# Kernel tuning notes

Measured on AMD Instinct MI355X. Metric: run time of the kernel, lower is better.

## Reference

```python
import jax, jax.numpy as jnp
import numpy as np

B = 4          # number of systems in batch
N_PER = 2000   # atoms per system (batch ids are sorted, equal-sized groups)
L = 20.0       # cubic cell edge length (Angstrom)
DL = 2.0       # grid resolution (module default)
SIGMA = 1.0    # Gaussian width (module default)
EPS = 1e-6
NORM = 90.0474
NK = int(np.floor(L / DL))  # static k-grid extent = floor(|cell row| / dl) = 10


def setup_inputs() -> dict:
    key = jax.random.key(0)
    k1, k2 = jax.random.split(key)
    r = jax.random.uniform(k1, (B * N_PER, 3), dtype=jnp.float32) * L
    q = jax.random.normal(k2, (B * N_PER, 1), dtype=jnp.float32)
    cell = jnp.tile(jnp.eye(3, dtype=jnp.float32)[None] * L, (B, 1, 1))
    batch = jnp.repeat(jnp.arange(B, dtype=jnp.int64), N_PER)
    return {"q": q, "r": r, "cell": cell, "batch": batch}


def _ewald(q, r, cell):
    twopi = 2.0 * np.pi
    k_sq_max = (twopi / DL) ** 2
    sigma_sq_half = SIGMA ** 2 / 2.0

    # Static integer k-grid n in [-NK, NK]^3, shape (K, 3), K = (2*NK+1)**3
    rng = jnp.arange(-NK, NK + 1, dtype=r.dtype)
    n1, n2, n3 = jnp.meshgrid(rng, rng, rng, indexing='ij')
    nvec = jnp.stack([n1.ravel(), n2.ravel(), n3.ravel()], axis=1)
    # Hemisphere filter: sign of first nonzero component of nvec > 0
    # (origin n==0 is excluded below by the k_sq > 0 mask, matching torch)
    hemi = ((nvec[:, 0] > 0)
            | ((nvec[:, 0] == 0) & (nvec[:, 1] > 0))
            | ((nvec[:, 0] == 0) & (nvec[:, 1] == 0) & (nvec[:, 2] > 0)))

    # Reciprocal lattice G = 2*pi * inv(cell)^T, per system
    G = twopi * jnp.linalg.inv(cell).transpose(0, 2, 1)        # (B, 3, 3)
    kvec = jnp.einsum('kd,bde->bke', nvec, G)                   # (B, K, 3)
    k_sq = jnp.sum(kvec ** 2, axis=-1)                          # (B, K)
    mask = (k_sq > 0) & (k_sq <= k_sq_max) & hemi[None, :]      # (B, K)

    kfac = jnp.exp(-sigma_sq_half * k_sq) / (k_sq + EPS)        # (B, K)

    pos_b = r.reshape(B, N_PER, 3)
    q_b = q.reshape(B, N_PER)

    kdr = jnp.einsum('bnd,bkd->bnk', pos_b, kvec)               # (B, N, K)
    S_real = jnp.einsum('bn,bnk->bk', q_b, jnp.cos(kdr))        # (B, K)
    S_imag = jnp.einsum('bn,bnk->bk', q_b, jnp.sin(kdr))        # (B, K)
    S_sq = S_real ** 2 + S_imag ** 2

    volume = jnp.linalg.det(cell)                               # (B,)
    # factor is 2.0 for every surviving k (origin masked out), matching torch
    pot = jnp.sum(jnp.where(mask, 2.0 * kfac * S_sq, 0.0), axis=1) / volume
    pot = pot - jnp.sum(q_b ** 2, axis=1) / (SIGMA * twopi ** 1.5)
    return pot * NORM                                           # (B,)


def reference(q, r, cell, batch):
    # batch ids are sorted with equal group sizes N_PER, so a reshape
    # reproduces the per-batch loop of the torch module exactly.
    return _ewald(q, r, cell)
```

## Files before the change

kernel.cpp:

```cpp
#include <hip/hip_runtime.h>
#include <math.h>

#define NSYS 4
#define NPER 2000
#define NKD 10
#define NCH 16
#define ACH (NPER / NCH)
#define TPB 256
#define RTPB 1024

#define TWOPI 6.28318530717958647692f
#define NORMC 90.0474f
#define SELFC 0.06349363593424097f
#define EPSV 1e-6f

constexpr int klist_count() {
    int c = 0;
    for (int nx = -NKD; nx <= NKD; ++nx)
        for (int ny = -NKD; ny <= NKD; ++ny)
            for (int nz = -NKD; nz <= NKD; ++nz) {
                bool hemi = (nx > 0) || (nx == 0 && ny > 0) ||
                            (nx == 0 && ny == 0 && nz > 0);
                if (hemi && nx*nx + ny*ny + nz*nz <= NKD*NKD) ++c;
            }
    return c;
}
constexpr int KACT = klist_count();
#define KBLKS ((KACT + TPB - 1) / TPB)
#define KACTP (KBLKS * TPB)

struct alignas(16) KTab { short v[KACT][4]; };
constexpr KTab make_ktab() {
    KTab t{};
    int c = 0;
    for (int nx = -NKD; nx <= NKD; ++nx)
        for (int ny = -NKD; ny <= NKD; ++ny)
            for (int nz = -NKD; nz <= NKD; ++nz) {
                bool hemi = (nx > 0) || (nx == 0 && ny > 0) ||
                            (nx == 0 && ny == 0 && nz > 0);
                if (hemi && nx*nx + ny*ny + nz*nz <= NKD*NKD) {
                    t.v[c][0] = (short)nx; t.v[c][1] = (short)ny;
                    t.v[c][2] = (short)nz; t.v[c][3] = 0;
                    ++c;
                }
            }
    return t;
}
__device__ const KTab g_ktab = make_ktab();

__device__ inline void invdet3(const float* __restrict__ c, float* inv, float& det) {
    float a00=c[0],a01=c[1],a02=c[2],a10=c[3],a11=c[4],a12=c[5],a20=c[6],a21=c[7],a22=c[8];
    float c00 = a11*a22 - a12*a21;
    float c01 = a12*a20 - a10*a22;
    float c02 = a10*a21 - a11*a20;
    det = a00*c00 + a01*c01 + a02*c02;
    float id = 1.0f / det;
    inv[0] = c00*id;
    inv[1] = (a02*a21 - a01*a22)*id;
    inv[2] = (a01*a12 - a02*a11)*id;
    inv[3] = c01*id;
    inv[4] = (a00*a22 - a02*a20)*id;
    inv[5] = (a02*a10 - a00*a12)*id;
    inv[6] = c02*id;
    inv[7] = (a01*a20 - a00*a21)*id;
    inv[8] = (a00*a11 - a01*a10)*id;
}

__device__ inline float hw_sin_rev(float t) {
#if __has_builtin(__builtin_amdgcn_sinf)
    return __builtin_amdgcn_sinf(t);
#else
    return __sinf(t * TWOPI);
#endif
}
__device__ inline float hw_cos_rev(float t) {
#if __has_builtin(__builtin_amdgcn_cosf)
    return __builtin_amdgcn_cosf(t);
#else
    return __cosf(t * TWOPI);
#endif
}

__global__ __launch_bounds__(TPB) void ewald_sk(
    const float* __restrict__ q, const float* __restrict__ r,
    const float* __restrict__ cell,
    float* __restrict__ ws_sr, float* __restrict__ ws_si)
{
    const int b  = blockIdx.z;
    const int ch = blockIdx.y;
    const int t  = blockIdx.x * TPB + threadIdx.x;

    __shared__ float4 s_at[ACH];

    float cl[9];
#pragma unroll
    for (int i = 0; i < 9; ++i) cl[i] = cell[b*9 + i];
    float inv[9], det;
    invdet3(cl, inv, det);

    const int a0 = b * NPER + ch * ACH;
    if (threadIdx.x < ACH) {
        int i = threadIdx.x;
        float x = r[(a0+i)*3 + 0];
        float y = r[(a0+i)*3 + 1];
        float z = r[(a0+i)*3 + 2];
        float t0 = inv[0]*x + inv[3]*y + inv[6]*z;
        float t1 = inv[1]*x + inv[4]*y + inv[7]*z;
        float t2 = inv[2]*x + inv[5]*y + inv[8]*z;
        s_at[i] = make_float4(t0, t1, t2, q[a0+i]);
    }
    __syncthreads();

    if (t < KACT) {
        const short4* kt = reinterpret_cast<const short4*>(g_ktab.v);
        short4 kk = kt[t];
        float fnx = (float)kk.x, fny = (float)kk.y, fnz = (float)kk.z;

        float Sr = 0.0f, Si = 0.0f;
#pragma unroll 5
        for (int i = 0; i < ACH; ++i) {
            float4 a = s_at[i];
            float rev = fmaf(fnx, a.x, fmaf(fny, a.y, fnz * a.z));
            float fr  = rev - floorf(rev);
            float sn  = hw_sin_rev(fr);
            float cs  = hw_cos_rev(fr);
            Sr = fmaf(a.w, cs, Sr);
            Si = fmaf(a.w, sn, Si);
        }
        int o = (b * NCH + ch) * KACTP + t;
        ws_sr[o] = Sr;
        ws_si[o] = Si;
    }
}

__global__ __launch_bounds__(RTPB) void ewald_reduce(
    const float* __restrict__ q, const float* __restrict__ cell,
    const float* __restrict__ ws_sr, const float* __restrict__ ws_si,
    float* __restrict__ out)
{
    const int b = blockIdx.x;

    float cl[9];
#pragma unroll
    for (int i = 0; i < 9; ++i) cl[i] = cell[b*9 + i];
    float inv[9], det;
    invdet3(cl, inv, det);

    const short4* kt = reinterpret_cast<const short4*>(g_ktab.v);

    float acc = 0.0f;
    for (int t = threadIdx.x; t < KACT; t += RTPB) {
        short4 kk = kt[t];
        float fnx = (float)kk.x, fny = (float)kk.y, fnz = (float)kk.z;
        float kv0 = TWOPI * (fnx*inv[0] + fny*inv[1] + fnz*inv[2]);
        float kv1 = TWOPI * (fnx*inv[3] + fny*inv[4] + fnz*inv[5]);
        float kv2 = TWOPI * (fnx*inv[6] + fny*inv[7] + fnz*inv[8]);
        float ksq = kv0*kv0 + kv1*kv1 + kv2*kv2;

        float Sr = 0.0f, Si = 0.0f;
#pragma unroll
        for (int ch = 0; ch < NCH; ++ch) {
            int o = (b * NCH + ch) * KACTP + t;
            Sr += ws_sr[o];
            Si += ws_si[o];
        }
        acc += __expf(-0.5f * ksq) / (ksq + EPSV) * (Sr*Sr + Si*Si);
    }

    float qs = 0.0f;
    for (int i = threadIdx.x; i < NPER; i += RTPB) {
        float qq = q[b * NPER + i];
        qs = fmaf(qq, qq, qs);
    }

#pragma unroll
    for (int off = 32; off > 0; off >>= 1) {
        acc += __shfl_down(acc, off);
        qs  += __shfl_down(qs,  off);
    }
    __shared__ float racc[RTPB/64], rqs[RTPB/64];
    int wid = threadIdx.x >> 6, lane = threadIdx.x & 63;
    if (lane == 0) { racc[wid] = acc; rqs[wid] = qs; }
    __syncthreads();
    if (threadIdx.x == 0) {
        float a = 0.0f, s = 0.0f;
#pragma unroll
        for (int w = 0; w < RTPB/64; ++w) { a += racc[w]; s += rqs[w]; }
        out[b] = (2.0f * a / det - s * SELFC) * NORMC;
    }
}

extern "C" void kernel_launch(void* const* d_in, const int* in_sizes, int n_in,
                              void* d_out, int out_size, void* d_ws, size_t ws_size,
                              hipStream_t stream) {
    const float* q    = (const float*)d_in[0];
    const float* r    = (const float*)d_in[1];
    const float* cell = (const float*)d_in[2];
    float* out = (float*)d_out;

    float* ws_sr = (float*)d_ws;
    float* ws_si = ws_sr + (size_t)NSYS * NCH * KACTP;

    dim3 g1(KBLKS, NCH, NSYS);
    ewald_sk<<<g1, TPB, 0, stream>>>(q, r, cell, ws_sr, ws_si);

    ewald_reduce<<<dim3(NSYS), RTPB, 0, stream>>>(q, cell, ws_sr, ws_si, out);
}
```

Baseline: 72.21 us.

## Fuse structure-factor and reduction kernels using per-block completion flags

```diff
diff --git a/kernel.cpp b/kernel.cpp
--- a/kernel.cpp
+++ b/kernel.cpp
@@ -7,12 +7,12 @@
 #define NCH 16
 #define ACH (NPER / NCH)
 #define TPB 256
-#define RTPB 1024
 
 #define TWOPI 6.28318530717958647692f
 #define NORMC 90.0474f
 #define SELFC 0.06349363593424097f
 #define EPSV 1e-6f
+#define MAGIC 0x5A3C7E1Fu
 
 constexpr int klist_count() {
     int c = 0;
@@ -28,6 +28,7 @@
 constexpr int KACT = klist_count();
 #define KBLKS ((KACT + TPB - 1) / TPB)
 #define KACTP (KBLKS * TPB)
+#define NFLG  (NCH * KBLKS)
 
 struct alignas(16) KTab { short v[KACT][4]; };
 constexpr KTab make_ktab() {
@@ -81,16 +82,14 @@
 #endif
 }
 
-__global__ __launch_bounds__(TPB) void ewald_sk(
+__global__ __launch_bounds__(TPB) void ewald_fused(
     const float* __restrict__ q, const float* __restrict__ r,
     const float* __restrict__ cell,
-    float* __restrict__ ws_sr, float* __restrict__ ws_si)
+    float* __restrict__ ws_sr, float* __restrict__ ws_si,
+    unsigned int* __restrict__ flags,
+    float* __restrict__ out)
 {
-    const int b  = blockIdx.z;
-    const int ch = blockIdx.y;
-    const int t  = blockIdx.x * TPB + threadIdx.x;
-
-    __shared__ float4 s_at[ACH];
+    const int b = blockIdx.z;
 
     float cl[9];
 #pragma unroll
@@ -98,58 +97,72 @@
     float inv[9], det;
     invdet3(cl, inv, det);
 
-    const int a0 = b * NPER + ch * ACH;
-    if (threadIdx.x < ACH) {
-        int i = threadIdx.x;
-        float x = r[(a0+i)*3 + 0];
-        float y = r[(a0+i)*3 + 1];
-        float z = r[(a0+i)*3 + 2];
-        float t0 = inv[0]*x + inv[3]*y + inv[6]*z;
-        float t1 = inv[1]*x + inv[4]*y + inv[7]*z;
-        float t2 = inv[2]*x + inv[5]*y + inv[8]*z;
-        s_at[i] = make_float4(t0, t1, t2, q[a0+i]);
-    }
-    __syncthreads();
-
-    if (t < KACT) {
-        const short4* kt = reinterpret_cast<const short4*>(g_ktab.v);
-        short4 kk = kt[t];
-        float fnx = (float)kk.x, fny = (float)kk.y, fnz = (float)kk.z;
-
-        float Sr = 0.0f, Si = 0.0f;
+    const short4* kt = reinterpret_cast<const short4*>(g_ktab.v);
+
+    if (blockIdx.y < NCH) {
+        const int ch = blockIdx.y;
+        const int t  = blockIdx.x * TPB + threadIdx.x;
+
+        __shared__ float4 s_at[ACH];
+
+        const int a0 = b * NPER + ch * ACH;
+        if (threadIdx.x < ACH) {
+            int i = threadIdx.x;
+            float x = r[(a0+i)*3 + 0];
+            float y = r[(a0+i)*3 + 1];
+            float z = r[(a0+i)*3 + 2];
+            float t0 = inv[0]*x + inv[3]*y + inv[6]*z;
+            float t1 = inv[1]*x + inv[4]*y + inv[7]*z;
+            float t2 = inv[2]*x + inv[5]*y + inv[8]*z;
+            s_at[i] = make_float4(t0, t1, t2, q[a0+i]);
+        }
+        __syncthreads();
+
+        if (t < KACT) {
+            short4 kk = kt[t];
+            float fnx = (float)kk.x, fny = (float)kk.y, fnz = (float)kk.z;
+            float Sr = 0.0f, Si = 0.0f;
 #pragma unroll 5
-        for (int i = 0; i < ACH; ++i) {
-            float4 a = s_at[i];
-            float rev = fmaf(fnx, a.x, fmaf(fny, a.y, fnz * a.z));
-            float fr  = rev - floorf(rev);
-            float sn  = hw_sin_rev(fr);
-            float cs  = hw_cos_rev(fr);
-            Sr = fmaf(a.w, cs, Sr);
-            Si = fmaf(a.w, sn, Si);
-        }
-        int o = (b * NCH + ch) * KACTP + t;
-        ws_sr[o] = Sr;
-        ws_si[o] = Si;
-    }
-}
-
-__global__ __launch_bounds__(RTPB) void ewald_reduce(
-    const float* __restrict__ q, const float* __restrict__ cell,
-    const float* __restrict__ ws_sr, const float* __restrict__ ws_si,
-    float* __restrict__ out)
-{
-    const int b = blockIdx.x;
-
-    float cl[9];
-#pragma unroll
-    for (int i = 0; i < 9; ++i) cl[i] = cell[b*9 + i];
-    float inv[9], det;
-    invdet3(cl, inv, det);
-
-    const short4* kt = reinterpret_cast<const short4*>(g_ktab.v);
+            for (int i = 0; i < ACH; ++i) {
+                float4 a = s_at[i];
+                float rev = fmaf(fnx, a.x, fmaf(fny, a.y, fnz * a.z));
+                float fr  = rev - floorf(rev);
+                float sn  = hw_sin_rev(fr);
+                float cs  = hw_cos_rev(fr);
+                Sr = fmaf(a.w, cs, Sr);
+                Si = fmaf(a.w, sn, Si);
+            }
+            int o = (b * NCH + ch) * KACTP + t;
+            ws_sr[o] = Sr;
+            ws_si[o] = Si;
+        }
+        __syncthreads();
+        if (threadIdx.x == 0) {
+            __threadfence();
+            __hip_atomic_store(&flags[b * NFLG + ch * KBLKS + blockIdx.x],
+                               MAGIC, __ATOMIC_RELAXED, __HIP_MEMORY_SCOPE_AGENT);
+        }
+        return;
+    }
+
+    if (blockIdx.x != 0) return;
+
+    {
+        const unsigned int* fb = flags + b * NFLG;
+        bool done = false;
+        for (long it = 0; it < (1L << 22) && !done; ++it) {
+            int ok = 1;
+            if (threadIdx.x < NFLG)
+                ok = (__hip_atomic_load(&fb[threadIdx.x], __ATOMIC_RELAXED,
+                                        __HIP_MEMORY_SCOPE_AGENT) == MAGIC);
+            done = __syncthreads_and(ok);
+            if (!done) __builtin_amdgcn_s_sleep(8);
+        }
+    }
+    __threadfence();
 
     float acc = 0.0f;
-    for (int t = threadIdx.x; t < KACT; t += RTPB) {
+    for (int t = threadIdx.x; t < KACT; t += TPB) {
         short4 kk = kt[t];
         float fnx = (float)kk.x, fny = (float)kk.y, fnz = (float)kk.z;
         float kv0 = TWOPI * (fnx*inv[0] + fny*inv[1] + fnz*inv[2]);
@@ -168,7 +181,7 @@
     }
 
     float qs = 0.0f;
-    for (int i = threadIdx.x; i < NPER; i += RTPB) {
+    for (int i = threadIdx.x; i < NPER; i += TPB) {
         float qq = q[b * NPER + i];
         qs = fmaf(qq, qq, qs);
     }
@@ -178,14 +191,14 @@
         acc += __shfl_down(acc, off);
         qs  += __shfl_down(qs,  off);
     }
-    __shared__ float racc[RTPB/64], rqs[RTPB/64];
+    __shared__ float racc[TPB/64], rqs[TPB/64];
     int wid = threadIdx.x >> 6, lane = threadIdx.x & 63;
     if (lane == 0) { racc[wid] = acc; rqs[wid] = qs; }
     __syncthreads();
     if (threadIdx.x == 0) {
         float a = 0.0f, s = 0.0f;
 #pragma unroll
-        for (int w = 0; w < RTPB/64; ++w) { a += racc[w]; s += rqs[w]; }
+        for (int w = 0; w < TPB/64; ++w) { a += racc[w]; s += rqs[w]; }
         out[b] = (2.0f * a / det - s * SELFC) * NORMC;
     }
 }
@@ -200,9 +213,8 @@
 
     float* ws_sr = (float*)d_ws;
     float* ws_si = ws_sr + (size_t)NSYS * NCH * KACTP;
-
-    dim3 g1(KBLKS, NCH, NSYS);
-    ewald_sk<<<g1, TPB, 0, stream>>>(q, r, cell, ws_sr, ws_si);
-
-    ewald_reduce<<<dim3(NSYS), RTPB, 0, stream>>>(q, cell, ws_sr, ws_si, out);
-}
+    unsigned int* flags = (unsigned int*)(ws_si + (size_t)NSYS * NCH * KACTP);
+
+    dim3 g(KBLKS, NCH + 1, NSYS);
+    ewald_fused<<<g, TPB, 0, stream>>>(q, r, cell, ws_sr, ws_si, flags, out);
+}
```

After: 88.20 us. +22.1%, slower.
